# Optimization experiments

Measured on AMD Instinct MI355X. Metric: run time of the kernel, lower is better.

## Reference

```python
import jax, jax.numpy as jnp
import numpy as np

N = 50000   # num_nodes
E = 1600000 # edges (avg degree 32)
D = 256     # in_feats
H = 256     # n_hidden


def setup_inputs() -> dict:
    key = jax.random.key(0)
    ks = jax.random.split(key, 9)
    s = 1.0 / np.sqrt(D)
    return {
        "input_nodes": jnp.arange(N, dtype=jnp.int32),
        "edge_src": jax.random.randint(ks[0], (E,), 0, N, dtype=jnp.int32),
        "edge_dst": jax.random.randint(ks[1], (E,), 0, N, dtype=jnp.int32),
        "emb": jax.random.normal(ks[2], (N, D), jnp.float32) * 0.02,
        "W_self0": jax.random.normal(ks[3], (D, H), jnp.float32) * s,
        "W_neigh0": jax.random.normal(ks[4], (D, H), jnp.float32) * s,
        "b0": jnp.zeros((H,), jnp.float32),
        "W_self1": jax.random.normal(ks[5], (H, H), jnp.float32) * s,
        "W_neigh1": jax.random.normal(ks[6], (H, H), jnp.float32) * s,
        "b1": jnp.zeros((H,), jnp.float32),
    }


def _sage_mean(h, src, dst, W_self, W_neigh, b, n):
    # gather neighbor features, mean-reduce by destination, then linear.
    msgs = h[src]                                                  # [E, d]
    ssum = jax.ops.segment_sum(msgs, dst, num_segments=n)          # [n, d]
    deg = jax.ops.segment_sum(jnp.ones(src.shape, h.dtype), dst, num_segments=n)
    h_neigh = ssum / jnp.maximum(deg, 1.0)[:, None]
    return h @ W_self + h_neigh @ W_neigh + b


def reference(input_nodes, edge_src, edge_dst, emb,
              W_self0, W_neigh0, b0, W_self1, W_neigh1, b1):
    h = emb[input_nodes]                                            # [N, D]
    h = _sage_mean(h, edge_src, edge_dst, W_self0, W_neigh0, b0, N)
    h = jax.nn.relu(h)  # dropout is identity at inference
    h = _sage_mean(h, edge_src, edge_dst, W_self1, W_neigh1, b1, N)
    h = h / jnp.linalg.norm(h)  # global Frobenius norm, as in torch.norm(h)
    return h
```

## Files before the change

### kernel.cpp

```cpp
#include <hip/hip_runtime.h>
#include <math.h>

#define NN 50000
#define NE 1600000
#define DF 256
#define NBUCK 391
#define CHS4 ((long long)NN * 64)
#define HALFN 25000

typedef unsigned short ushortT;
typedef __attribute__((ext_vector_type(8))) short short8;
typedef __attribute__((ext_vector_type(4))) float floatx4;
typedef __attribute__((ext_vector_type(4))) unsigned uintx4;

__device__ __forceinline__ unsigned bf16rne(float f) {
    unsigned u = __float_as_uint(f);
    return (u + 0x7fffu + ((u >> 16) & 1u)) >> 16;
}

#define ASYNC16(gptr, ldsptr) \
    __builtin_amdgcn_global_load_lds((const __attribute__((address_space(1))) unsigned*)(gptr), \
                                     (__attribute__((address_space(3))) unsigned*)(ldsptr), 16, 0, 0)


__global__ __launch_bounds__(256)
void k_bhist(const int* __restrict__ dst, int* __restrict__ bcnt) {
    __shared__ int h[NBUCK];
    for (int i = threadIdx.x; i < NBUCK; i += 256) h[i] = 0;
    __syncthreads();
    int base = blockIdx.x * 4096;
#pragma unroll
    for (int i = 0; i < 16; ++i) {
        int e = base + i * 256 + threadIdx.x;
        if (e < NE) atomicAdd(&h[dst[e] >> 7], 1);
    }
    __syncthreads();
    for (int i = threadIdx.x; i < NBUCK; i += 256)
        if (h[i]) atomicAdd(&bcnt[i], h[i]);
}

__global__ void k_bscan(const int* __restrict__ bcnt, int* __restrict__ bbase,
                        int* __restrict__ cursor, int* __restrict__ row_ptr,
                        float* __restrict__ nrm) {
    __shared__ int s[512];
    int t = threadIdx.x;
    int v = (t < NBUCK) ? bcnt[t] : 0;
    s[t] = v; __syncthreads();
    for (int off = 1; off < 512; off <<= 1) {
        int x = (t >= off) ? s[t - off] : 0;
        __syncthreads();
        s[t] += x;
        __syncthreads();
    }
    if (t < NBUCK) { bbase[t] = s[t] - v; cursor[t] = s[t] - v; }
    if (t == 0) { bbase[NBUCK] = NE; row_ptr[NN] = NE; *nrm = 0.0f; }
}

__global__ __launch_bounds__(256)
void k_bin(const int* __restrict__ src, const int* __restrict__ dst,
           int* __restrict__ cursor, unsigned* __restrict__ rec) {
    __shared__ int h[NBUCK];
    __shared__ int gb[NBUCK];
    for (int i = threadIdx.x; i < NBUCK; i += 256) h[i] = 0;
    __syncthreads();
    const int base = blockIdx.x * 2048;
    int bk[8], rk[8];
    unsigned pk[8];
#pragma unroll
    for (int i = 0; i < 8; ++i) {
        int e = base + i * 256 + threadIdx.x;
        if (e < NE) {
            int d = dst[e];
            bk[i] = d >> 7;
            pk[i] = (unsigned)src[e] | ((unsigned)(d & 127) << 16);
            rk[i] = atomicAdd(&h[bk[i]], 1);
        } else bk[i] = -1;
    }
    __syncthreads();
    for (int i = threadIdx.x; i < NBUCK; i += 256) {
        int c = h[i];
        gb[i] = c ? atomicAdd(&cursor[i], c) : 0;
    }
    __syncthreads();
#pragma unroll
    for (int i = 0; i < 8; ++i)
        if (bk[i] >= 0) rec[gb[bk[i]] + rk[i]] = pk[i];
}


__global__ __launch_bounds__(256)
void k_csr(const unsigned* __restrict__ rec, const int* __restrict__ bbase,
           int* __restrict__ row_ptr, int* __restrict__ hp, ushortT* __restrict__ csr) {
    __shared__ int cnt[256];
    __shared__ int cur[256];
    __shared__ int s[256];
    const int B = blockIdx.x, t = threadIdx.x;
    cnt[t] = 0;
    __syncthreads();
    const int beg = bbase[B], end = bbase[B + 1];
    for (int p = beg + t; p < end; p += 256) {
        unsigned r = rec[p];
        int idx = (int)((r >> 16) & 127) * 2 + ((r & 0xffffu) >= HALFN ? 1 : 0);
        atomicAdd(&cnt[idx], 1);
    }
    __syncthreads();
    int v = cnt[t];
    s[t] = v; __syncthreads();
    for (int off = 1; off < 256; off <<= 1) {
        int x = (t >= off) ? s[t - off] : 0;
        __syncthreads();
        s[t] += x;
        __syncthreads();
    }
    cur[t] = s[t] - v;
    __syncthreads();
    if (t < 128) {
        int node = B * 128 + t;
        if (node < NN) {
            row_ptr[node] = beg + s[2 * t] - cnt[2 * t];
            hp[node]      = beg + s[2 * t + 1] - cnt[2 * t + 1];
        }
    }
    for (int p = beg + t; p < end; p += 256) {
        unsigned r = rec[p];
        int idx = (int)((r >> 16) & 127) * 2 + ((r & 0xffffu) >= HALFN ? 1 : 0);
        int loc = atomicAdd(&cur[idx], 1);
        csr[beg + loc] = (ushortT)r;
    }
}


__global__ __launch_bounds__(256)
void k_cvt(const float* __restrict__ emb, const int* __restrict__ gather,
           ushortT* __restrict__ embb,
           const float* __restrict__ Ws0, const float* __restrict__ Wn0,
           ushortT* __restrict__ Wt0,
           const float* __restrict__ Ws1, const float* __restrict__ Wn1,
           ushortT* __restrict__ Wt1) {
    const int b = blockIdx.x;
    if (b < 6250) {
        long long i = ((long long)b * 256 + threadIdx.x) * 8;
        int row = (int)(i >> 8);
        int col = (int)(i & 255);
        long long g = (long long)gather[row] * 256 + col;
        float4 v0 = *(const float4*)(emb + g);
        float4 v1 = *(const float4*)(emb + g + 4);
        uint4 o;
        o.x = bf16rne(v0.x) | (bf16rne(v0.y) << 16);
        o.y = bf16rne(v0.z) | (bf16rne(v0.w) << 16);
        o.z = bf16rne(v1.x) | (bf16rne(v1.y) << 16);
        o.w = bf16rne(v1.z) | (bf16rne(v1.w) << 16);
        *(uint4*)(embb + ((long long)(col >> 6) * NN + row) * 64 + (col & 63)) = o;
    } else {
        const bool first = b < 6762;
        const int idx = ((first ? b - 6250 : b - 6762)) * 256 + threadIdx.x;
        const int n = idx >> 9;
        const int k = idx & 511;
        const float* Ws = first ? Ws0 : Ws1;
        const float* Wn = first ? Wn0 : Wn1;
        float v = (k < 256) ? Ws[k * 256 + n] : Wn[(k - 256) * 256 + n];
        (first ? Wt0 : Wt1)[idx] = (ushortT)bf16rne(v);
    }
}


__global__ __launch_bounds__(256)
void k_agg(const ushortT* __restrict__ feat, const int* __restrict__ row_ptr,
           const ushortT* __restrict__ csr, ushortT* __restrict__ out) {
    const int c    = blockIdx.x & 3;
    const int ng   = blockIdx.x >> 2;
    const int node = ng * 32 + (threadIdx.x >> 3);
    const int part = (threadIdx.x & 7) * 8;
    if (node >= NN) return;

    const ushortT* fc = feat + (long long)c * CHS4;
    const int beg = row_ptr[node], end = row_ptr[node + 1];

    float s[8] = {0.f, 0.f, 0.f, 0.f, 0.f, 0.f, 0.f, 0.f};

#define ACCUM(q) do { \
        s[0] += __uint_as_float(q.x << 16); \
        s[1] += __uint_as_float(q.x & 0xffff0000u); \
        s[2] += __uint_as_float(q.y << 16); \
        s[3] += __uint_as_float(q.y & 0xffff0000u); \
        s[4] += __uint_as_float(q.z << 16); \
        s[5] += __uint_as_float(q.z & 0xffff0000u); \
        s[6] += __uint_as_float(q.w << 16); \
        s[7] += __uint_as_float(q.w & 0xffff0000u); \
    } while (0)

    int p = beg;

    if (p < end && (p & 1)) {
        int i0 = (int)__builtin_nontemporal_load(csr + p);
        uintx4 q = *(const uintx4*)(fc + i0 * 64 + part);
        ACCUM(q);
        ++p;
    }

    unsigned x0 = 0, x1 = 0, x2 = 0, x3 = 0;
    if (p + 7 < end) {
        const unsigned* cp = (const unsigned*)(csr + p);
        x0 = __builtin_nontemporal_load(cp + 0);
        x1 = __builtin_nontemporal_load(cp + 1);
        x2 = __builtin_nontemporal_load(cp + 2);
        x3 = __builtin_nontemporal_load(cp + 3);
    }

    while (p + 7 < end) {
        uintx4 q0 = *(const uintx4*)(fc + (int)(x0 & 0xffffu) * 64 + part);
        uintx4 q1 = *(const uintx4*)(fc + (int)(x0 >> 16)     * 64 + part);
        uintx4 q2 = *(const uintx4*)(fc + (int)(x1 & 0xffffu) * 64 + part);
        uintx4 q3 = *(const uintx4*)(fc + (int)(x1 >> 16)     * 64 + part);
        uintx4 q4 = *(const uintx4*)(fc + (int)(x2 & 0xffffu) * 64 + part);
        uintx4 q5 = *(const uintx4*)(fc + (int)(x2 >> 16)     * 64 + part);
        uintx4 q6 = *(const uintx4*)(fc + (int)(x3 & 0xffffu) * 64 + part);
        uintx4 q7 = *(const uintx4*)(fc + (int)(x3 >> 16)     * 64 + part);

        const int np = p + 8;
        if (np + 7 < end) {
            const unsigned* cp = (const unsigned*)(csr + np);
            x0 = __builtin_nontemporal_load(cp + 0);
            x1 = __builtin_nontemporal_load(cp + 1);
            x2 = __builtin_nontemporal_load(cp + 2);
            x3 = __builtin_nontemporal_load(cp + 3);
        }

        ACCUM(q0); ACCUM(q1); ACCUM(q2); ACCUM(q3);
        ACCUM(q4); ACCUM(q5); ACCUM(q6); ACCUM(q7);
        p = np;
    }

    for (; p < end; ++p) {
        int i0 = (int)__builtin_nontemporal_load(csr + p);
        uintx4 q = *(const uintx4*)(fc + i0 * 64 + part);
        ACCUM(q);
    }
#undef ACCUM

    float inv = 1.0f / fmaxf((float)(end - beg), 1.0f);
    uintx4 o;
    o.x = bf16rne(s[0] * inv) | (bf16rne(s[1] * inv) << 16);
    o.y = bf16rne(s[2] * inv) | (bf16rne(s[3] * inv) << 16);
    o.z = bf16rne(s[4] * inv) | (bf16rne(s[5] * inv) << 16);
    o.w = bf16rne(s[6] * inv) | (bf16rne(s[7] * inv) << 16);
    __builtin_nontemporal_store(o, (uintx4*)(out + ((long long)c * NN + node) * 64 + part));
}


template<int RELU, int NORM>
__global__ __launch_bounds__(512, 4)
void k_gemm(const ushortT* __restrict__ Aself, const ushortT* __restrict__ Aneigh,
            const ushortT* __restrict__ Wt, const float* __restrict__ bias,
            ushortT* __restrict__ Cb, float* __restrict__ Cf, float* __restrict__ norm_acc) {
    __shared__ ushortT LDSBUF[12288];
    __shared__ float red[8];
    ushortT* As = LDSBUF;
    ushortT* Bs = LDSBUF + 4096;

    const int t = threadIdx.x;
    const int w = t >> 6;
    const int lane = t & 63;
    const int wm = w >> 2;
    const int wn = w & 3;
    const int m0 = blockIdx.x * 128;

    const int ar = t >> 2;
    const int cu = (t & 3) * 8;

    const long long gA = (long long)min(m0 + ar, NN - 1) * 64 + cu;

    const unsigned ldsA = w * 512;
    const unsigned ldsB = w * 512;

    const int fm = lane & 15;
    const int fk = (lane >> 4) * 8;

    floatx4 acc[4][4];
#pragma unroll
    for (int i = 0; i < 4; ++i)
#pragma unroll
        for (int j = 0; j < 4; ++j) acc[i][j] = (floatx4){0.f, 0.f, 0.f, 0.f};

    for (int kt = 0; kt < 512; kt += 32) {
        const int kc = (kt < 256) ? kt : kt - 256;
        const ushortT* Ab = ((kt < 256) ? Aself : Aneigh)
                          + (long long)(kc >> 6) * CHS4 + (kc & 32);

        __syncthreads();
        ASYNC16(Ab + gA, As + ldsA);
#pragma unroll
        for (int i = 0; i < 2; ++i)
            ASYNC16(Wt + (i * 128 + ar) * 512 + kt + cu, Bs + i * 4096 + ldsB);
        __syncthreads();

        short8 af[4], bf[4];
#pragma unroll
        for (int i = 0; i < 4; ++i)
            af[i] = *(const short8*)&As[(wm * 64 + i * 16 + fm) * 32 + fk];
#pragma unroll
        for (int j = 0; j < 4; ++j)
            bf[j] = *(const short8*)&Bs[(wn * 64 + j * 16 + fm) * 32 + fk];
#pragma unroll
        for (int i = 0; i < 4; ++i)
#pragma unroll
            for (int j = 0; j < 4; ++j)
                acc[i][j] = __builtin_amdgcn_mfma_f32_16x16x32_bf16(af[i], bf[j], acc[i][j], 0, 0, 0);
    }

    float bj[4];
#pragma unroll
    for (int j = 0; j < 4; ++j) bj[j] = bias[wn * 64 + j * 16 + fm];

    __syncthreads();

    if (!NORM) {
        ushortT (*Cs)[256] = (ushortT(*)[256])LDSBUF;
#pragma unroll
        for (int g = 0; g < 4; ++g) {
            if (wm == (g >> 1)) {
#pragma unroll
                for (int ii = 0; ii < 2; ++ii) {
                    const int i = (g & 1) * 2 + ii;
#pragma unroll
                    for (int r = 0; r < 4; ++r) {
                        const int lrow = ii * 16 + (lane >> 4) * 4 + r;
#pragma unroll
                        for (int j = 0; j < 4; ++j) {
                            const int col = wn * 64 + j * 16 + fm;
                            float v = acc[i][j][r] + bj[j];
                            if (RELU) v = fmaxf(v, 0.0f);
                            Cs[lrow][col] = (ushortT)bf16rne(v);
                        }
                    }
                }
            }
            __syncthreads();
#pragma unroll
            for (int siter = 0; siter < 2; ++siter) {
                const int id = t + siter * 512;
                const int k8 = id & 7;
                const int cc = (id >> 3) & 3;
                const int lr = id >> 5;
                const int R = m0 + g * 32 + lr;
                if (R < NN) {
                    uintx4 val = *(const uintx4*)&Cs[lr][cc * 64 + k8 * 8];
                    *(uintx4*)(Cb + ((long long)cc * NN + R) * 64 + k8 * 8) = val;
                }
            }
            __syncthreads();
        }
    } else {
        float (*Csf)[256] = (float(*)[256])LDSBUF;
        float sumsq = 0.0f;
#pragma unroll
        for (int g = 0; g < 8; ++g) {
            if (wm == (g >> 2)) {
                const int i = g & 3;
#pragma unroll
                for (int r = 0; r < 4; ++r) {
                    const int lrow = (lane >> 4) * 4 + r;
#pragma unroll
                    for (int j = 0; j < 4; ++j) {
                        const int col = wn * 64 + j * 16 + fm;
                        Csf[lrow][col] = acc[i][j][r] + bj[j];
                    }
                }
            }
            __syncthreads();
#pragma unroll
            for (int siter = 0; siter < 2; ++siter) {
                const int id = t + siter * 512;
                const int lr = id >> 6;
                const int k  = id & 63;
                const int R = m0 + g * 16 + lr;
                if (R < NN) {
                    float4 val = *(const float4*)&Csf[lr][k * 4];
                    sumsq += val.x * val.x + val.y * val.y + val.z * val.z + val.w * val.w;
                    *(float4*)(Cf + (long long)R * 256 + k * 4) = val;
                }
            }
            __syncthreads();
        }
#pragma unroll
        for (int off = 32; off > 0; off >>= 1) sumsq += __shfl_down(sumsq, off);
        if (lane == 0) red[w] = sumsq;
        __syncthreads();
        if (t == 0) {
            float tot = 0.f;
#pragma unroll
            for (int i = 0; i < 8; ++i) tot += red[i];
            atomicAdd(norm_acc, tot);
        }
    }
}

__global__ void k_scale(float* __restrict__ out, const float* __restrict__ nrm) {
    const float s = 1.0f / sqrtf(*nrm);
    long long i = ((long long)blockIdx.x * 256 + threadIdx.x) * 4;
    float4 v = *(float4*)&out[i];
    v.x *= s; v.y *= s; v.z *= s; v.w *= s;
    *(float4*)&out[i] = v;
}


extern "C" void kernel_launch(void* const* d_in, const int* in_sizes, int n_in,
                              void* d_out, int out_size, void* d_ws, size_t ws_size,
                              hipStream_t stream) {
    const int*   input_nodes = (const int*)d_in[0];
    const int*   esrc = (const int*)d_in[1];
    const int*   edst = (const int*)d_in[2];
    const float* emb  = (const float*)d_in[3];
    const float* Ws0  = (const float*)d_in[4];
    const float* Wn0  = (const float*)d_in[5];
    const float* b0   = (const float*)d_in[6];
    const float* Ws1  = (const float*)d_in[7];
    const float* Wn1  = (const float*)d_in[8];
    const float* b1   = (const float*)d_in[9];
    float* out = (float*)d_out;

    char* base = (char*)d_ws;
    ushortT*  embb    = (ushortT*) (base);
    ushortT*  h1b     = (ushortT*) (base + 25600000);
    ushortT*  hnb     = (ushortT*) (base + 51200000);
    unsigned* rec     = (unsigned*)(base + 76800000);
    ushortT*  csr     = (ushortT*) (base + 83200000);
    ushortT*  Wt0     = (ushortT*) (base + 86400000);
    ushortT*  Wt1     = (ushortT*) (base + 86662144);
    int*      row_ptr = (int*)     (base + 86924288);
    int*      hp      = (int*)     (base + 87124304);
    int*      bcnt    = (int*)     (base + 87324304);
    int*      bbase   = (int*)     (base + 87325904);
    int*      cursor  = (int*)     (base + 87327504);
    float*    nrm     = (float*)   (base + 87329104);

    hipMemsetAsync(bcnt, 0, NBUCK * sizeof(int), stream);
    k_bhist <<<391,   256, 0, stream>>>(edst, bcnt);
    k_bscan <<<1,     512, 0, stream>>>(bcnt, bbase, cursor, row_ptr, nrm);
    k_bin   <<<782,   256, 0, stream>>>(esrc, edst, cursor, rec);
    k_csr   <<<NBUCK, 256, 0, stream>>>(rec, bbase, row_ptr, hp, csr);

    k_cvt<<<7274, 256, 0, stream>>>(emb, input_nodes, embb, Ws0, Wn0, Wt0, Ws1, Wn1, Wt1);

    const int GEMM_BLOCKS = (NN + 127) / 128;
    const int AGG_BLOCKS  = ((NN + 31) / 32) * 4;

    k_agg<<<AGG_BLOCKS, 256, 0, stream>>>(embb, row_ptr, csr, hnb);
    k_gemm<1, 0><<<GEMM_BLOCKS, 512, 0, stream>>>(embb, hnb, Wt0, b0, h1b, nullptr, nullptr);

    k_agg<<<AGG_BLOCKS, 256, 0, stream>>>(h1b, row_ptr, csr, hnb);
    k_gemm<0, 1><<<GEMM_BLOCKS, 512, 0, stream>>>(h1b, hnb, Wt1, b1, nullptr, out, nrm);

    k_scale<<<NN * DF / 4 / 256, 256, 0, stream>>>(out, nrm);
}
```

Before: 437.0 us.

## Merge CSR build with bf16 conversion and shrink GEMM M-tile to 96 rows

The CSR-building kernel and the embedding/weight conversion kernel are merged into one launch, with the first NBUCK blocks doing CSR work and the rest doing conversion. This removes a launch boundary and lets the two independent jobs overlap. The GEMM row tile drops from 128 to 96, giving more blocks (about 521 versus 391) to fill the CUs better. The epilogue LDS rows are padded (264/260) to reduce bank conflicts. The trade-off is less reuse of the weight tile per block, since B is reloaded for fewer A rows.

Result: slower. 456.0 us (+4.4%).

```diff
diff --git a/kernel.cpp b/kernel.cpp
--- a/kernel.cpp
+++ b/kernel.cpp
@@ -89,57 +89,60 @@
 
 
 __global__ __launch_bounds__(256)
-void k_csr(const unsigned* __restrict__ rec, const int* __restrict__ bbase,
-           int* __restrict__ row_ptr, int* __restrict__ hp, ushortT* __restrict__ csr) {
+void k_csrcvt(const unsigned* __restrict__ rec, const int* __restrict__ bbase,
+              int* __restrict__ row_ptr, int* __restrict__ hp, ushortT* __restrict__ csr,
+              const float* __restrict__ emb, const int* __restrict__ gather,
+              ushortT* __restrict__ embb,
+              const float* __restrict__ Ws0, const float* __restrict__ Wn0,
+              ushortT* __restrict__ Wt0,
+              const float* __restrict__ Ws1, const float* __restrict__ Wn1,
+              ushortT* __restrict__ Wt1) {
     __shared__ int cnt[256];
     __shared__ int cur[256];
     __shared__ int s[256];
-    const int B = blockIdx.x, t = threadIdx.x;
-    cnt[t] = 0;
-    __syncthreads();
-    const int beg = bbase[B], end = bbase[B + 1];
-    for (int p = beg + t; p < end; p += 256) {
-        unsigned r = rec[p];
-        int idx = (int)((r >> 16) & 127) * 2 + ((r & 0xffffu) >= HALFN ? 1 : 0);
-        atomicAdd(&cnt[idx], 1);
-    }
-    __syncthreads();
-    int v = cnt[t];
-    s[t] = v; __syncthreads();
-    for (int off = 1; off < 256; off <<= 1) {
-        int x = (t >= off) ? s[t - off] : 0;
-        __syncthreads();
-        s[t] += x;
-        __syncthreads();
-    }
-    cur[t] = s[t] - v;
-    __syncthreads();
-    if (t < 128) {
-        int node = B * 128 + t;
-        if (node < NN) {
-            row_ptr[node] = beg + s[2 * t] - cnt[2 * t];
-            hp[node]      = beg + s[2 * t + 1] - cnt[2 * t + 1];
-        }
-    }
-    for (int p = beg + t; p < end; p += 256) {
-        unsigned r = rec[p];
-        int idx = (int)((r >> 16) & 127) * 2 + ((r & 0xffffu) >= HALFN ? 1 : 0);
-        int loc = atomicAdd(&cur[idx], 1);
-        csr[beg + loc] = (ushortT)r;
-    }
-}
-
-
-__global__ __launch_bounds__(256)
-void k_cvt(const float* __restrict__ emb, const int* __restrict__ gather,
-           ushortT* __restrict__ embb,
-           const float* __restrict__ Ws0, const float* __restrict__ Wn0,
-           ushortT* __restrict__ Wt0,
-           const float* __restrict__ Ws1, const float* __restrict__ Wn1,
-           ushortT* __restrict__ Wt1) {
-    const int b = blockIdx.x;
+    const int blk = blockIdx.x;
+    const int t = threadIdx.x;
+
+    if (blk < NBUCK) {
+        const int B = blk;
+        cnt[t] = 0;
+        __syncthreads();
+        const int beg = bbase[B], end = bbase[B + 1];
+        for (int p = beg + t; p < end; p += 256) {
+            unsigned r = rec[p];
+            int idx = (int)((r >> 16) & 127) * 2 + ((r & 0xffffu) >= HALFN ? 1 : 0);
+            atomicAdd(&cnt[idx], 1);
+        }
+        __syncthreads();
+        int v = cnt[t];
+        s[t] = v; __syncthreads();
+        for (int off = 1; off < 256; off <<= 1) {
+            int x = (t >= off) ? s[t - off] : 0;
+            __syncthreads();
+            s[t] += x;
+            __syncthreads();
+        }
+        cur[t] = s[t] - v;
+        __syncthreads();
+        if (t < 128) {
+            int node = B * 128 + t;
+            if (node < NN) {
+                row_ptr[node] = beg + s[2 * t] - cnt[2 * t];
+                hp[node]      = beg + s[2 * t + 1] - cnt[2 * t + 1];
+            }
+        }
+        for (int p = beg + t; p < end; p += 256) {
+            unsigned r = rec[p];
+            int idx = (int)((r >> 16) & 127) * 2 + ((r & 0xffffu) >= HALFN ? 1 : 0);
+            int loc = atomicAdd(&cur[idx], 1);
+            csr[beg + loc] = (ushortT)r;
+        }
+        return;
+    }
+
+    const int b = blk - NBUCK;
     if (b < 6250) {
-        long long i = ((long long)b * 256 + threadIdx.x) * 8;
+        long long i = ((long long)b * 256 + t) * 8;
         int row = (int)(i >> 8);
         int col = (int)(i & 255);
         long long g = (long long)gather[row] * 256 + col;
@@ -153,7 +156,7 @@
         *(uint4*)(embb + ((long long)(col >> 6) * NN + row) * 64 + (col & 63)) = o;
     } else {
         const bool first = b < 6762;
-        const int idx = ((first ? b - 6250 : b - 6762)) * 256 + threadIdx.x;
+        const int idx = ((first ? b - 6250 : b - 6762)) * 256 + t;
         const int n = idx >> 9;
         const int k = idx & 511;
         const float* Ws = first ? Ws0 : Ws1;
@@ -253,17 +256,17 @@
 void k_gemm(const ushortT* __restrict__ Aself, const ushortT* __restrict__ Aneigh,
             const ushortT* __restrict__ Wt, const float* __restrict__ bias,
             ushortT* __restrict__ Cb, float* __restrict__ Cf, float* __restrict__ norm_acc) {
-    __shared__ ushortT LDSBUF[12288];
+    __shared__ __align__(16) ushortT LDSBUF[12672];
     __shared__ float red[8];
     ushortT* As = LDSBUF;
-    ushortT* Bs = LDSBUF + 4096;
+    ushortT* Bs = LDSBUF + 3072;
 
     const int t = threadIdx.x;
     const int w = t >> 6;
     const int lane = t & 63;
     const int wm = w >> 2;
     const int wn = w & 3;
-    const int m0 = blockIdx.x * 128;
+    const int m0 = blockIdx.x * 96;
 
     const int ar = t >> 2;
     const int cu = (t & 3) * 8;
@@ -276,9 +279,9 @@
     const int fm = lane & 15;
     const int fk = (lane >> 4) * 8;
 
-    floatx4 acc[4][4];
-#pragma unroll
-    for (int i = 0; i < 4; ++i)
+    floatx4 acc[3][4];
+#pragma unroll
+    for (int i = 0; i < 3; ++i)
 #pragma unroll
         for (int j = 0; j < 4; ++j) acc[i][j] = (floatx4){0.f, 0.f, 0.f, 0.f};
 
@@ -288,21 +291,21 @@
                           + (long long)(kc >> 6) * CHS4 + (kc & 32);
 
         __syncthreads();
-        ASYNC16(Ab + gA, As + ldsA);
+        if (t < 384) ASYNC16(Ab + gA, As + ldsA);
 #pragma unroll
         for (int i = 0; i < 2; ++i)
             ASYNC16(Wt + (i * 128 + ar) * 512 + kt + cu, Bs + i * 4096 + ldsB);
         __syncthreads();
 
-        short8 af[4], bf[4];
-#pragma unroll
-        for (int i = 0; i < 4; ++i)
-            af[i] = *(const short8*)&As[(wm * 64 + i * 16 + fm) * 32 + fk];
+        short8 af[3], bf[4];
+#pragma unroll
+        for (int i = 0; i < 3; ++i)
+            af[i] = *(const short8*)&As[(wm * 48 + i * 16 + fm) * 32 + fk];
 #pragma unroll
         for (int j = 0; j < 4; ++j)
             bf[j] = *(const short8*)&Bs[(wn * 64 + j * 16 + fm) * 32 + fk];
 #pragma unroll
-        for (int i = 0; i < 4; ++i)
+        for (int i = 0; i < 3; ++i)
 #pragma unroll
             for (int j = 0; j < 4; ++j)
                 acc[i][j] = __builtin_amdgcn_mfma_f32_16x16x32_bf16(af[i], bf[j], acc[i][j], 0, 0, 0);
@@ -315,16 +318,15 @@
     __syncthreads();
 
     if (!NORM) {
-        ushortT (*Cs)[256] = (ushortT(*)[256])LDSBUF;
-#pragma unroll
-        for (int g = 0; g < 4; ++g) {
-            if (wm == (g >> 1)) {
-#pragma unroll
-                for (int ii = 0; ii < 2; ++ii) {
-                    const int i = (g & 1) * 2 + ii;
+        ushortT (*Cs)[264] = (ushortT(*)[264])LDSBUF;
+#pragma unroll
+        for (int g = 0; g < 2; ++g) {
+            if (wm == g) {
+#pragma unroll
+                for (int i = 0; i < 3; ++i)
 #pragma unroll
                     for (int r = 0; r < 4; ++r) {
-                        const int lrow = ii * 16 + (lane >> 4) * 4 + r;
+                        const int lrow = i * 16 + (lane >> 4) * 4 + r;
 #pragma unroll
                         for (int j = 0; j < 4; ++j) {
                             const int col = wn * 64 + j * 16 + fm;
@@ -333,38 +335,36 @@
                             Cs[lrow][col] = (ushortT)bf16rne(v);
                         }
                     }
+            }
+            __syncthreads();
+#pragma unroll
+            for (int siter = 0; siter < 3; ++siter) {
+                const int id = t + siter * 512;
+                const int lr = id >> 5;
+                const int sl = id & 31;
+                const int cc = sl >> 3;
+                const int q  = sl & 7;
+                const int R  = m0 + g * 48 + lr;
+                if (R < NN) {
+                    uintx4 val = *(const uintx4*)&Cs[lr][cc * 64 + q * 8];
+                    *(uintx4*)(Cb + ((long long)cc * NN + R) * 64 + q * 8) = val;
                 }
             }
             __syncthreads();
-#pragma unroll
-            for (int siter = 0; siter < 2; ++siter) {
-                const int id = t + siter * 512;
-                const int k8 = id & 7;
-                const int cc = (id >> 3) & 3;
-                const int lr = id >> 5;
-                const int R = m0 + g * 32 + lr;
-                if (R < NN) {
-                    uintx4 val = *(const uintx4*)&Cs[lr][cc * 64 + k8 * 8];
-                    *(uintx4*)(Cb + ((long long)cc * NN + R) * 64 + k8 * 8) = val;
-                }
-            }
-            __syncthreads();
         }
     } else {
-        float (*Csf)[256] = (float(*)[256])LDSBUF;
+        float (*Csf)[260] = (float(*)[260])LDSBUF;
         float sumsq = 0.0f;
 #pragma unroll
-        for (int g = 0; g < 8; ++g) {
-            if (wm == (g >> 2)) {
-                const int i = g & 3;
+        for (int g = 0; g < 6; ++g) {
+            if (wm == g / 3) {
+                const int i = g % 3;
 #pragma unroll
                 for (int r = 0; r < 4; ++r) {
                     const int lrow = (lane >> 4) * 4 + r;
 #pragma unroll
-                    for (int j = 0; j < 4; ++j) {
-                        const int col = wn * 64 + j * 16 + fm;
-                        Csf[lrow][col] = acc[i][j][r] + bj[j];
-                    }
+                    for (int j = 0; j < 4; ++j)
+                        Csf[lrow][wn * 64 + j * 16 + fm] = acc[i][j][r] + bj[j];
                 }
             }
             __syncthreads();
@@ -373,7 +373,7 @@
                 const int id = t + siter * 512;
                 const int lr = id >> 6;
                 const int k  = id & 63;
-                const int R = m0 + g * 16 + lr;
+                const int R  = m0 + (g / 3) * 48 + (g % 3) * 16 + lr;
                 if (R < NN) {
                     float4 val = *(const float4*)&Csf[lr][k * 4];
                     sumsq += val.x * val.x + val.y * val.y + val.z * val.z + val.w * val.w;
@@ -438,11 +438,12 @@
     k_bhist <<<391,   256, 0, stream>>>(edst, bcnt);
     k_bscan <<<1,     512, 0, stream>>>(bcnt, bbase, cursor, row_ptr, nrm);
     k_bin   <<<782,   256, 0, stream>>>(esrc, edst, cursor, rec);
-    k_csr   <<<NBUCK, 256, 0, stream>>>(rec, bbase, row_ptr, hp, csr);
-
-    k_cvt<<<7274, 256, 0, stream>>>(emb, input_nodes, embb, Ws0, Wn0, Wt0, Ws1, Wn1, Wt1);
-
-    const int GEMM_BLOCKS = (NN + 127) / 128;
+
+    k_csrcvt<<<NBUCK + 7274, 256, 0, stream>>>(rec, bbase, row_ptr, hp, csr,
+                                               emb, input_nodes, embb,
+                                               Ws0, Wn0, Wt0, Ws1, Wn1, Wt1);
+
+    const int GEMM_BLOCKS = (NN + 95) / 96;
     const int AGG_BLOCKS  = ((NN + 31) / 32) * 4;
 
     k_agg<<<AGG_BLOCKS, 256, 0, stream>>>(embb, row_ptr, csr, hnb);
```
